# Performance work log

Measured on AMD Instinct MI355X. Metric: run time of the kernel, lower is better.

The kernel has to match this reference:

```python
import jax, jax.numpy as jnp
import numpy as np

B, L, QD, KVD, H = 8, 1024, 1024, 768, 16
DH = QD // H
EPS = 1e-5


def setup_inputs() -> dict:
    key = jax.random.key(0)
    ks = jax.random.split(key, 12)
    q = jax.random.normal(ks[0], (B, L, QD), jnp.float32)
    k = jax.random.normal(ks[1], (B, L, KVD), jnp.float32)
    v = jax.random.normal(ks[2], (B, L, KVD), jnp.float32)
    # key_padding_mask: True = valid token (code masks where ~mask)
    lengths = jax.random.randint(ks[3], (B,), L // 2, L + 1)
    key_padding_mask = jnp.arange(L)[None, :] < lengths[:, None]
    def lin(kk, fan_in, fan_out):
        bound = 1.0 / np.sqrt(fan_in)
        k1, k2 = jax.random.split(kk)
        W = jax.random.uniform(k1, (fan_out, fan_in), jnp.float32, -bound, bound)
        b = jax.random.uniform(k2, (fan_out,), jnp.float32, -bound, bound)
        return W, b
    Wq, bq = lin(ks[4], QD, QD)
    Wk, bk = lin(ks[5], KVD, QD)
    Wv, bv = lin(ks[6], KVD, QD)
    Wo, bo = lin(ks[7], QD, QD)
    gamma = jnp.ones((QD,), jnp.float32)
    beta = jnp.zeros((QD,), jnp.float32)
    return {"q": q, "k": k, "v": v, "key_padding_mask": key_padding_mask,
            "Wq": Wq, "bq": bq, "Wk": Wk, "bk": bk, "Wv": Wv, "bv": bv,
            "Wo": Wo, "bo": bo, "gamma": gamma, "beta": beta}


def reference(q, k, v, key_padding_mask, Wq, bq, Wk, bk, Wv, bv, Wo, bo, gamma, beta):
    Bq, Lq, C = q.shape
    scale = DH ** -0.5
    # projections -> [B, H, L, DH]
    qh = (q @ Wq.T + bq).reshape(Bq, Lq, H, DH).transpose(0, 2, 1, 3)
    kh = (k @ Wk.T + bk).reshape(Bq, Lq, H, DH).transpose(0, 2, 1, 3)
    vh = (v @ Wv.T + bv).reshape(Bq, Lq, H, DH).transpose(0, 2, 1, 3)
    attn = jnp.einsum('bhld,bhmd->bhlm', qh, kh) * scale
    attn = jnp.where(key_padding_mask[:, None, None, :], attn, -jnp.inf)
    p = jax.nn.softmax(attn, axis=-1)
    out = jnp.einsum('bhlm,bhmd->bhld', p, vh).transpose(0, 2, 1, 3).reshape(Bq, Lq, C)
    out = out @ Wo.T + bo  # dropout is identity in eval
    y = out + q
    mu = jnp.mean(y, axis=-1, keepdims=True)
    var = jnp.var(y, axis=-1, keepdims=True)
    return (y - mu) * jax.lax.rsqrt(var + EPS) * gamma + beta
```

## Files before the change

### kernel.cpp

```cpp
#include <hip/hip_runtime.h>
#include <stdint.h>

typedef float f32x4 __attribute__((ext_vector_type(4)));
typedef __bf16 bf16x8 __attribute__((ext_vector_type(8)));
typedef unsigned short u16;

__device__ __forceinline__ void gload_lds16(const void* g, void* l) {
  __builtin_amdgcn_global_load_lds(
      (__attribute__((address_space(1))) void*)(uintptr_t)(g),
      (__attribute__((address_space(3))) void*)(uint32_t)(uintptr_t)(l),
      16, 0, 0);
}

__device__ __forceinline__ u16 f2bf(float x) {
  __bf16 h = (__bf16)x;
  return *(u16*)&h;
}

__device__ __forceinline__ void barrier_raw() {
  __builtin_amdgcn_sched_barrier(0);
  __builtin_amdgcn_s_barrier();
  __builtin_amdgcn_sched_barrier(0);
}

#define VMCNT(n) asm volatile("s_waitcnt vmcnt(" #n ")" ::: "memory")
#define LGKM0()                                    \
  do {                                             \
    asm volatile("s_waitcnt lgkmcnt(0)" ::: "memory"); \
    __builtin_amdgcn_sched_barrier(0);             \
  } while (0)

__global__ __launch_bounds__(256) void cast_all(
    const float* __restrict__ q, const float* __restrict__ k,
    const float* __restrict__ v, const float* __restrict__ wq,
    const float* __restrict__ wk, const float* __restrict__ wv,
    const float* __restrict__ wo, u16* __restrict__ out) {
  const int g = blockIdx.x;
  const float* in;
  int s;
  if (g < 8192) { in = q; s = 0; }
  else if (g < 14336) { in = k; s = 8192; }
  else if (g < 20480) { in = v; s = 14336; }
  else if (g < 21504) { in = wq; s = 20480; }
  else if (g < 22272) { in = wk; s = 21504; }
  else if (g < 23040) { in = wv; s = 22272; }
  else { in = wo; s = 23040; }
  const int li = (g - s) * 256 + threadIdx.x;
  float4 x = *((const float4*)in + li);
  unsigned lo = (unsigned)f2bf(x.x) | ((unsigned)f2bf(x.y) << 16);
  unsigned hi = (unsigned)f2bf(x.z) | ((unsigned)f2bf(x.w) << 16);
  ((uint2*)out)[(size_t)g * 256 + threadIdx.x] = make_uint2(lo, hi);
}

__global__ __launch_bounds__(256, 2) void proj_kernel(
    const u16* __restrict__ qb, const u16* __restrict__ kb,
    const u16* __restrict__ vb, const u16* __restrict__ wqb,
    const u16* __restrict__ wkb, const u16* __restrict__ wvb,
    const float* __restrict__ bq, const float* __restrict__ bk,
    const float* __restrict__ bv, u16* __restrict__ qpb,
    u16* __restrict__ kpb, u16* __restrict__ vtb) {
  __shared__ __align__(16) u16 As[3][256 * 32];
  __shared__ __align__(16) u16 Bs[3][128 * 32];
  const int tid = threadIdx.x;
  const int role = blockIdx.y >> 3;
  const int m0 = blockIdx.x * 256, n0 = (blockIdx.y & 7) * 128;
  const int K = (role == 0) ? 1024 : 768;
  const u16* A = (role == 0) ? qb : ((role == 1) ? kb : vb);
  const u16* Bt = (role == 0) ? wqb : ((role == 1) ? wkb : wvb);
  const float* bias = (role == 0) ? bq : ((role == 1) ? bk : bv);
  const int lane = tid & 63, w = tid >> 6;
  const int wr = w >> 1, wc = w & 1;
  const int l16 = lane & 15, lk = lane >> 4;
  const int nk = K >> 5;
  const int srow = tid >> 2;
  const int sw = (tid & 3) ^ ((tid >> 3) & 3);
  const int e2 = (l16 >> 1) & 3;

  const u16* Ap = A + (size_t)(m0 + srow) * K + sw * 8;
  const u16* Bp = Bt + (size_t)(n0 + srow) * K + sw * 8;

  f32x4 acc[8][4] = {};
  bf16x8 aA[8], bA[4], aB[8], bB[4];

  auto stage = [&](int t, int ktile) {
    const int ko = ktile << 5;
#pragma unroll
    for (int l = 0; l < 4; ++l)
      gload_lds16(Ap + (size_t)l * 64 * K + ko, As[t] + tid * 8 + l * 2048);
#pragma unroll
    for (int l = 0; l < 2; ++l)
      gload_lds16(Bp + (size_t)l * 64 * K + ko, Bs[t] + tid * 8 + l * 2048);
  };
  auto rd = [&](bf16x8 (&a)[8], bf16x8 (&b)[4], int c) {
#pragma unroll
    for (int i = 0; i < 8; ++i)
      a[i] = *(const bf16x8*)(As[c] + (wr * 128 + i * 16 + l16) * 32 + (lk ^ e2) * 8);
#pragma unroll
    for (int j = 0; j < 4; ++j)
      b[j] = *(const bf16x8*)(Bs[c] + (wc * 64 + j * 16 + l16) * 32 + (lk ^ e2) * 8);
  };
  auto mm = [&](bf16x8 (&a)[8], bf16x8 (&b)[4]) {
    __builtin_amdgcn_s_setprio(1);
#pragma unroll
    for (int i = 0; i < 8; ++i)
#pragma unroll
      for (int j = 0; j < 4; ++j)
        acc[i][j] = __builtin_amdgcn_mfma_f32_16x16x32_bf16(a[i], b[j], acc[i][j], 0, 0, 0);
    __builtin_amdgcn_s_setprio(0);
  };

  stage(0, 0);
  stage(1, 1);
  VMCNT(6);
  barrier_raw();
  rd(aA, bA, 0);
  LGKM0();

  int cur = 0;
  for (int kt = 0; kt < nk; kt += 2) {
    const int c1 = (cur == 2) ? 0 : cur + 1;
    const int c2 = (c1 == 2) ? 0 : c1 + 1;
    if (kt + 2 < nk) { stage(c2, kt + 2); VMCNT(6); }
    else { VMCNT(0); }
    barrier_raw();
    rd(aB, bB, c1);
    mm(aA, bA);
    LGKM0();
    barrier_raw();
    if (kt + 3 < nk) { stage(cur, kt + 3); VMCNT(6); }
    else { VMCNT(0); }
    barrier_raw();
    if (kt + 2 < nk) rd(aA, bA, c2);
    mm(aB, bB);
    LGKM0();
    barrier_raw();
    cur = c2;
  }

#pragma unroll
  for (int i = 0; i < 8; ++i) {
    const int mrow = m0 + wr * 128 + i * 16 + lk * 4;
#pragma unroll
    for (int j = 0; j < 4; ++j) {
      const int col = n0 + wc * 64 + j * 16 + l16;
      const float bval = bias[col];
      if (role == 0) {
#pragma unroll
        for (int r = 0; r < 4; ++r)
          qpb[(size_t)(mrow + r) * 1024 + col] = f2bf(acc[i][j][r] + bval);
      } else if (role == 1) {
#pragma unroll
        for (int r = 0; r < 4; ++r)
          kpb[(size_t)(mrow + r) * 1024 + col] = f2bf(acc[i][j][r] + bval);
      } else {
        const int bb = mrow >> 10, l = mrow & 1023;
        const int hh = col >> 6, dd = col & 63;
        u16 u0 = f2bf(acc[i][j][0] + bval);
        u16 u1 = f2bf(acc[i][j][1] + bval);
        u16 u2 = f2bf(acc[i][j][2] + bval);
        u16 u3 = f2bf(acc[i][j][3] + bval);
        uint2 pkt = make_uint2((unsigned)u0 | ((unsigned)u1 << 16),
                               (unsigned)u2 | ((unsigned)u3 << 16));
        *(uint2*)(vtb + ((size_t)((bb * 16 + hh) * 64 + dd) << 10) + l) = pkt;
      }
    }
  }
}

__global__ __launch_bounds__(256) void attn_kernel(
    const u16* __restrict__ qp, const u16* __restrict__ kp,
    const u16* __restrict__ vt, const int* __restrict__ mask,
    u16* __restrict__ out) {
  __shared__ __align__(16) u16 KV[2][2][64 * 64];
  __shared__ __align__(16) u16 Ps[4][16 * 64];
  const int tid = threadIdx.x;
  const int qt = blockIdx.x, h = blockIdx.y, b = blockIdx.z;
  const int lane = tid & 63, w = tid >> 6;
  const int l16 = lane & 15, lk = lane >> 4;
  const int srow = tid >> 3, schunk = tid & 7;
  const int sw = schunk ^ (srow & 7);

  int cnt = 0;
  {
    const int4* mp = (const int4*)(mask + (b << 10));
#pragma unroll
    for (int i = 0; i < 4; ++i) {
      const int4 mv = mp[lane * 4 + i];
      cnt += (mv.x ? 1 : 0) + (mv.y ? 1 : 0) + (mv.z ? 1 : 0) + (mv.w ? 1 : 0);
    }
#pragma unroll
    for (int off = 1; off < 64; off <<= 1) cnt += __shfl_xor(cnt, off);
  }
  const int ntile = (cnt + 63) >> 6;
  const int rem = cnt & 63;

#pragma unroll
  for (int p = 0; p < 2; ++p) {
    gload_lds16(qp + (((size_t)(b * 1024 + qt * 64 + p * 32 + srow)) << 10) + h * 64 + sw * 8,
                KV[1][0] + tid * 8 + p * 2048);
    gload_lds16(kp + (((size_t)(b * 1024 + p * 32 + srow)) << 10) + h * 64 + sw * 8,
                KV[0][0] + tid * 8 + p * 2048);
    gload_lds16(vt + (((size_t)((b * 16 + h) * 64 + p * 32 + srow)) << 10) + sw * 8,
                KV[0][1] + tid * 8 + p * 2048);
  }
  __syncthreads();
  const int qrow = w * 16 + l16, qs = qrow & 7;
  bf16x8 aq0 = *(const bf16x8*)(KV[1][0] + qrow * 64 + (lk ^ qs) * 8);
  bf16x8 aq1 = *(const bf16x8*)(KV[1][0] + qrow * 64 + ((lk + 4) ^ qs) * 8);
  __syncthreads();

  const float SC2 = 0.18033688011112042f;
  float lsumq = 0.f;
  f32x4 oacc[4] = {};
  const int e7 = l16 & 7;

  int cur = 0;
  for (int kt = 0; kt < ntile; ++kt) {
    if (kt + 1 < ntile) {
#pragma unroll
      for (int p = 0; p < 2; ++p) {
        gload_lds16(kp + (((size_t)(b * 1024 + (kt + 1) * 64 + p * 32 + srow)) << 10) + h * 64 + sw * 8,
                    KV[cur ^ 1][0] + tid * 8 + p * 2048);
        gload_lds16(vt + (((size_t)((b * 16 + h) * 64 + p * 32 + srow)) << 10) + (kt + 1) * 64 + sw * 8,
                    KV[cur ^ 1][1] + tid * 8 + p * 2048);
      }
    }
    const u16* Kb = KV[cur][0];
    const u16* Vb = KV[cur][1];

    f32x4 sfr[4] = {};
    __builtin_amdgcn_s_setprio(1);
#pragma unroll
    for (int nf = 0; nf < 4; ++nf) {
      const int krow = nf * 16 + l16;
      bf16x8 bk0 = *(const bf16x8*)(Kb + krow * 64 + (lk ^ e7) * 8);
      bf16x8 bk1 = *(const bf16x8*)(Kb + krow * 64 + ((lk + 4) ^ e7) * 8);
      sfr[nf] = __builtin_amdgcn_mfma_f32_16x16x32_bf16(bk0, aq0, sfr[nf], 0, 0, 0);
      sfr[nf] = __builtin_amdgcn_mfma_f32_16x16x32_bf16(bk1, aq1, sfr[nf], 0, 0, 0);
    }
    __builtin_amdgcn_s_setprio(0);

    const bool partial = (kt == ntile - 1) && (rem != 0);
    u16* Pw = &Ps[w][0];
#pragma unroll
    for (int nf = 0; nf < 4; ++nf) {
      float pv0 = __builtin_amdgcn_exp2f(sfr[nf][0] * SC2);
      float pv1 = __builtin_amdgcn_exp2f(sfr[nf][1] * SC2);
      float pv2 = __builtin_amdgcn_exp2f(sfr[nf][2] * SC2);
      float pv3 = __builtin_amdgcn_exp2f(sfr[nf][3] * SC2);
      if (partial) {
        const int k0 = nf * 16 + lk * 4;
        pv0 = (k0 + 0 < rem) ? pv0 : 0.f;
        pv1 = (k0 + 1 < rem) ? pv1 : 0.f;
        pv2 = (k0 + 2 < rem) ? pv2 : 0.f;
        pv3 = (k0 + 3 < rem) ? pv3 : 0.f;
      }
      lsumq += (pv0 + pv1) + (pv2 + pv3);
      unsigned lo = (unsigned)f2bf(pv0) | ((unsigned)f2bf(pv1) << 16);
      unsigned hi = (unsigned)f2bf(pv2) | ((unsigned)f2bf(pv3) << 16);
      *(uint2*)(Pw + l16 * 64 + (((nf * 2 + (lk >> 1)) ^ e7) * 8 + (lk & 1) * 4)) =
          make_uint2(lo, hi);
    }

    bf16x8 ap0 = *(const bf16x8*)(Pw + l16 * 64 + ((lk ^ e7) * 8));
    bf16x8 ap1 = *(const bf16x8*)(Pw + l16 * 64 + (((4 + lk) ^ e7) * 8));
    __builtin_amdgcn_s_setprio(1);
#pragma unroll
    for (int nf = 0; nf < 4; ++nf) {
      const int vrow = nf * 16 + l16;
      bf16x8 bv0 = *(const bf16x8*)(Vb + vrow * 64 + (lk ^ e7) * 8);
      bf16x8 bv1 = *(const bf16x8*)(Vb + vrow * 64 + ((lk + 4) ^ e7) * 8);
      oacc[nf] = __builtin_amdgcn_mfma_f32_16x16x32_bf16(ap0, bv0, oacc[nf], 0, 0, 0);
      oacc[nf] = __builtin_amdgcn_mfma_f32_16x16x32_bf16(ap1, bv1, oacc[nf], 0, 0, 0);
    }
    __builtin_amdgcn_s_setprio(0);

    __syncthreads();
    cur ^= 1;
  }

  lsumq += __shfl_xor(lsumq, 16);
  lsumq += __shfl_xor(lsumq, 32);
  float rinv[4];
#pragma unroll
  for (int r = 0; r < 4; ++r) rinv[r] = 1.0f / __shfl(lsumq, lk * 4 + r);

#pragma unroll
  for (int nf = 0; nf < 4; ++nf)
#pragma unroll
    for (int r = 0; r < 4; ++r) {
      const int tok = b * 1024 + qt * 64 + w * 16 + lk * 4 + r;
      const int col = h * 64 + nf * 16 + l16;
      out[((size_t)tok << 10) + col] = f2bf(oacc[nf][r] * rinv[r]);
    }
}

__global__ __launch_bounds__(256, 3) void gemm_o(
    const u16* __restrict__ A, const u16* __restrict__ Bt,
    const float* __restrict__ bias, float* __restrict__ Cf,
    const float* __restrict__ res) {
  __shared__ __align__(16) u16 As[3][128 * 32];
  __shared__ __align__(16) u16 Bs[3][128 * 32];
  const int K = 1024, N = 1024, nk = 32;
  const int tid = threadIdx.x;
  const int m0 = blockIdx.x * 128, n0 = blockIdx.y * 128;
  const int lane = tid & 63, w = tid >> 6;
  const int wr = w >> 1, wc = w & 1;
  const int l16 = lane & 15, lk = lane >> 4;
  const int srow = tid >> 2;
  const int sw = (tid & 3) ^ ((tid >> 3) & 3);
  const int e2 = (l16 >> 1) & 3;

  const u16* Ap = A + (size_t)(m0 + srow) * K + sw * 8;
  const u16* Bp = Bt + (size_t)(n0 + srow) * K + sw * 8;

  f32x4 acc[4][4] = {};
  bf16x8 aA[4], bA[4], aB[4], bB[4];

  auto stage = [&](int t, int ktile) {
    const int ko = ktile << 5;
#pragma unroll
    for (int p = 0; p < 2; ++p) {
      gload_lds16(Ap + (size_t)p * 64 * K + ko, As[t] + tid * 8 + p * 2048);
      gload_lds16(Bp + (size_t)p * 64 * K + ko, Bs[t] + tid * 8 + p * 2048);
    }
  };
  auto rd = [&](bf16x8 (&a)[4], bf16x8 (&b)[4], int c) {
#pragma unroll
    for (int i = 0; i < 4; ++i)
      a[i] = *(const bf16x8*)(As[c] + (wr * 64 + i * 16 + l16) * 32 + (lk ^ e2) * 8);
#pragma unroll
    for (int j = 0; j < 4; ++j)
      b[j] = *(const bf16x8*)(Bs[c] + (wc * 64 + j * 16 + l16) * 32 + (lk ^ e2) * 8);
  };
  auto mm = [&](bf16x8 (&a)[4], bf16x8 (&b)[4]) {
    __builtin_amdgcn_s_setprio(1);
#pragma unroll
    for (int i = 0; i < 4; ++i)
#pragma unroll
      for (int j = 0; j < 4; ++j)
        acc[i][j] = __builtin_amdgcn_mfma_f32_16x16x32_bf16(a[i], b[j], acc[i][j], 0, 0, 0);
    __builtin_amdgcn_s_setprio(0);
  };

  stage(0, 0);
  stage(1, 1);
  VMCNT(4);
  barrier_raw();
  rd(aA, bA, 0);
  LGKM0();

  int cur = 0;
  for (int kt = 0; kt < nk; kt += 2) {
    const int c1 = (cur == 2) ? 0 : cur + 1;
    const int c2 = (c1 == 2) ? 0 : c1 + 1;
    if (kt + 2 < nk) { stage(c2, kt + 2); VMCNT(4); }
    else { VMCNT(0); }
    barrier_raw();
    rd(aB, bB, c1);
    mm(aA, bA);
    LGKM0();
    barrier_raw();
    if (kt + 3 < nk) { stage(cur, kt + 3); VMCNT(4); }
    else { VMCNT(0); }
    barrier_raw();
    if (kt + 2 < nk) rd(aA, bA, c2);
    mm(aB, bB);
    LGKM0();
    barrier_raw();
    cur = c2;
  }

#pragma unroll
  for (int i = 0; i < 4; ++i) {
    const int mrow = m0 + wr * 64 + i * 16 + lk * 4;
#pragma unroll
    for (int j = 0; j < 4; ++j) {
      const int col = n0 + wc * 64 + j * 16 + l16;
      const float bval = bias[col];
#pragma unroll
      for (int r = 0; r < 4; ++r) {
        const size_t idx = (size_t)(mrow + r) * N + col;
        Cf[idx] = acc[i][j][r] + bval + res[idx];
      }
    }
  }
}

__global__ __launch_bounds__(256) void ln_kernel(float* __restrict__ y,
                                                 const float* __restrict__ gamma,
                                                 const float* __restrict__ beta) {
  __shared__ float ssum[4], ssq[4];
  const int tid = threadIdx.x;
  float* yr = y + ((size_t)blockIdx.x << 10);
  float4 v = *((const float4*)yr + tid);
  float s = v.x + v.y + v.z + v.w;
  float q2 = v.x * v.x + v.y * v.y + v.z * v.z + v.w * v.w;
#pragma unroll
  for (int off = 1; off < 64; off <<= 1) {
    s += __shfl_xor(s, off);
    q2 += __shfl_xor(q2, off);
  }
  if ((tid & 63) == 0) { ssum[tid >> 6] = s; ssq[tid >> 6] = q2; }
  __syncthreads();
  s = ssum[0] + ssum[1] + ssum[2] + ssum[3];
  q2 = ssq[0] + ssq[1] + ssq[2] + ssq[3];
  const float mu = s * (1.0f / 1024.0f);
  const float rstd = rsqrtf(q2 * (1.0f / 1024.0f) - mu * mu + 1e-5f);
  float4 g = *((const float4*)gamma + tid);
  float4 be = *((const float4*)beta + tid);
  float4 o;
  o.x = (v.x - mu) * rstd * g.x + be.x;
  o.y = (v.y - mu) * rstd * g.y + be.y;
  o.z = (v.z - mu) * rstd * g.z + be.z;
  o.w = (v.w - mu) * rstd * g.w + be.w;
  *((float4*)yr + tid) = o;
}

extern "C" void kernel_launch(void* const* d_in, const int* in_sizes, int n_in,
                              void* d_out, int out_size, void* d_ws, size_t ws_size,
                              hipStream_t stream) {
  (void)in_sizes; (void)n_in; (void)out_size; (void)ws_size;
  const float* q = (const float*)d_in[0];
  const float* k = (const float*)d_in[1];
  const float* v = (const float*)d_in[2];
  const int* msk = (const int*)d_in[3];
  const float* Wq = (const float*)d_in[4];
  const float* bq = (const float*)d_in[5];
  const float* Wk = (const float*)d_in[6];
  const float* bk = (const float*)d_in[7];
  const float* Wv = (const float*)d_in[8];
  const float* bv = (const float*)d_in[9];
  const float* Wo = (const float*)d_in[10];
  const float* bo = (const float*)d_in[11];
  const float* gamma = (const float*)d_in[12];
  const float* beta = (const float*)d_in[13];
  float* out = (float*)d_out;

  char* p = (char*)d_ws;
  auto take = [&p](size_t bytes) {
    char* r = p;
    p += (bytes + 255) & ~(size_t)255;
    return r;
  };
  u16* qb = (u16*)take(8192ull * 1024 * 2);
  u16* kb = (u16*)take(8192ull * 768 * 2);
  u16* vb = (u16*)take(8192ull * 768 * 2);
  u16* wqb = (u16*)take(1024ull * 1024 * 2);
  u16* wkb = (u16*)take(1024ull * 768 * 2);
  u16* wvb = (u16*)take(1024ull * 768 * 2);
  u16* wob = (u16*)take(1024ull * 1024 * 2);
  u16* qpb = (u16*)take(8192ull * 1024 * 2);
  u16* kpb = (u16*)take(8192ull * 1024 * 2);
  u16* vtb = (u16*)take(8192ull * 1024 * 2);
  u16* atb = (u16*)take(8192ull * 1024 * 2);

  cast_all<<<dim3(24064), 256, 0, stream>>>(q, k, v, Wq, Wk, Wv, Wo, qb);

  proj_kernel<<<dim3(32, 24), 256, 0, stream>>>(qb, kb, vb, wqb, wkb, wvb,
                                                bq, bk, bv, qpb, kpb, vtb);

  attn_kernel<<<dim3(16, 16, 8), 256, 0, stream>>>(qpb, kpb, vtb, msk, atb);

  gemm_o<<<dim3(64, 8), 256, 0, stream>>>(atb, wob, bo, out, q);

  ln_kernel<<<dim3(8192), 256, 0, stream>>>(out, gamma, beta);
}
```

Baseline: 199.0 us.

## Simplify projection GEMM pipeline and remap attention grid for L2 locality

The projection GEMM drops its double-register ping-pong loop with split LDS reads, and replaces it with a single-stage-per-iteration loop over a three-buffer LDS ring. Each iteration keeps two tiles in flight using explicit vmcnt waits. The attention kernel moves to a 1D grid with swizzled block-to-(b,h,qt) mapping, so that blocks for the same head run close together and share K/V in cache. The trade-off is less overlap between LDS reads and MFMA in the GEMM, in exchange for fewer barriers per k-tile.

Result: faster. 175.3 us (-11.9%).

```diff
diff --git a/kernel.cpp b/kernel.cpp
--- a/kernel.cpp
+++ b/kernel.cpp
@@ -74,16 +74,13 @@
   const int nk = K >> 5;
   const int srow = tid >> 2;
   const int sw = (tid & 3) ^ ((tid >> 3) & 3);
-  const int e2 = (l16 >> 1) & 3;
 
   const u16* Ap = A + (size_t)(m0 + srow) * K + sw * 8;
   const u16* Bp = Bt + (size_t)(n0 + srow) * K + sw * 8;
 
   f32x4 acc[8][4] = {};
-  bf16x8 aA[8], bA[4], aB[8], bB[4];
-
-  auto stage = [&](int t, int ktile) {
-    const int ko = ktile << 5;
+
+  auto stage = [&](int t, int ko) {
 #pragma unroll
     for (int l = 0; l < 4; ++l)
       gload_lds16(Ap + (size_t)l * 64 * K + ko, As[t] + tid * 8 + l * 2048);
@@ -91,15 +88,31 @@
     for (int l = 0; l < 2; ++l)
       gload_lds16(Bp + (size_t)l * 64 * K + ko, Bs[t] + tid * 8 + l * 2048);
   };
-  auto rd = [&](bf16x8 (&a)[8], bf16x8 (&b)[4], int c) {
+
+  stage(0, 0);
+  stage(1, 32);
+
+  const int e2 = (l16 >> 1) & 3;
+  int cur = 0;
+  for (int kt = 0; kt < nk; ++kt) {
+    const int stg = (cur >= 1) ? cur - 1 : 2;
+    if (kt + 2 < nk) {
+      stage(stg, (kt + 2) << 5);
+      asm volatile("s_waitcnt vmcnt(12)" ::: "memory");
+    } else if (kt + 1 < nk) {
+      asm volatile("s_waitcnt vmcnt(6)" ::: "memory");
+    } else {
+      asm volatile("s_waitcnt vmcnt(0)" ::: "memory");
+    }
+    barrier_raw();
+
+    bf16x8 a[8], b[4];
 #pragma unroll
     for (int i = 0; i < 8; ++i)
-      a[i] = *(const bf16x8*)(As[c] + (wr * 128 + i * 16 + l16) * 32 + (lk ^ e2) * 8);
+      a[i] = *(const bf16x8*)(As[cur] + (wr * 128 + i * 16 + l16) * 32 + (lk ^ e2) * 8);
 #pragma unroll
     for (int j = 0; j < 4; ++j)
-      b[j] = *(const bf16x8*)(Bs[c] + (wc * 64 + j * 16 + l16) * 32 + (lk ^ e2) * 8);
-  };
-  auto mm = [&](bf16x8 (&a)[8], bf16x8 (&b)[4]) {
+      b[j] = *(const bf16x8*)(Bs[cur] + (wc * 64 + j * 16 + l16) * 32 + (lk ^ e2) * 8);
     __builtin_amdgcn_s_setprio(1);
 #pragma unroll
     for (int i = 0; i < 8; ++i)
@@ -107,34 +120,8 @@
       for (int j = 0; j < 4; ++j)
         acc[i][j] = __builtin_amdgcn_mfma_f32_16x16x32_bf16(a[i], b[j], acc[i][j], 0, 0, 0);
     __builtin_amdgcn_s_setprio(0);
-  };
-
-  stage(0, 0);
-  stage(1, 1);
-  VMCNT(6);
-  barrier_raw();
-  rd(aA, bA, 0);
-  LGKM0();
-
-  int cur = 0;
-  for (int kt = 0; kt < nk; kt += 2) {
-    const int c1 = (cur == 2) ? 0 : cur + 1;
-    const int c2 = (c1 == 2) ? 0 : c1 + 1;
-    if (kt + 2 < nk) { stage(c2, kt + 2); VMCNT(6); }
-    else { VMCNT(0); }
-    barrier_raw();
-    rd(aB, bB, c1);
-    mm(aA, bA);
-    LGKM0();
-    barrier_raw();
-    if (kt + 3 < nk) { stage(cur, kt + 3); VMCNT(6); }
-    else { VMCNT(0); }
-    barrier_raw();
-    if (kt + 2 < nk) rd(aA, bA, c2);
-    mm(aB, bB);
-    LGKM0();
-    barrier_raw();
-    cur = c2;
+    barrier_raw();
+    cur = (cur < 2) ? cur + 1 : 0;
   }
 
 #pragma unroll
@@ -174,7 +161,10 @@
   __shared__ __align__(16) u16 KV[2][2][64 * 64];
   __shared__ __align__(16) u16 Ps[4][16 * 64];
   const int tid = threadIdx.x;
-  const int qt = blockIdx.x, h = blockIdx.y, b = blockIdx.z;
+  const int bid = blockIdx.x;
+  const int qt = (bid >> 3) & 15;
+  const int bh = (bid & 7) + ((bid >> 7) << 3);
+  const int b = bh >> 4, h = bh & 15;
   const int lane = tid & 63, w = tid >> 6;
   const int l16 = lane & 15, lk = lane >> 4;
   const int srow = tid >> 3, schunk = tid & 7;
@@ -460,7 +450,7 @@
   proj_kernel<<<dim3(32, 24), 256, 0, stream>>>(qb, kb, vb, wqb, wkb, wvb,
                                                 bq, bk, bv, qpb, kpb, vtb);
 
-  attn_kernel<<<dim3(16, 16, 8), 256, 0, stream>>>(qpb, kpb, vtb, msk, atb);
+  attn_kernel<<<dim3(2048), 256, 0, stream>>>(qpb, kpb, vtb, msk, atb);
 
   gemm_o<<<dim3(64, 8), 256, 0, stream>>>(atb, wob, bo, out, q);
 
```
